# Performance work log

Measured on AMD Instinct MI355X. Metric: run time of the kernel, lower is better.

Reference implementation:

```python
import jax, jax.numpy as jnp
import numpy as np

N_NODES = 50000
N_EDGES = 1600000
IN_C = 256
HID_C = 128
OUT_C = 16
HEADS = 8
NEG_SLOPE = 0.2  # PyG GATConv default


def gat_layer(x, src, dst, W, att_src, att_dst, bias, heads, out_c):
    """PyG-style GATConv (eval mode, add_self_loops already applied to src/dst).
    x: [N, F_in], W: [F_in, heads*out_c], att_*: [heads, out_c], bias: [heads*out_c].
    Returns concatenated heads: [N, heads*out_c]."""
    N = x.shape[0]
    h = (x @ W).reshape(N, heads, out_c)                  # [N, H, C]
    a_src = (h * att_src[None]).sum(-1)                   # [N, H]
    a_dst = (h * att_dst[None]).sum(-1)                   # [N, H]
    alpha = a_src[src] + a_dst[dst]                       # [E, H]
    alpha = jax.nn.leaky_relu(alpha, NEG_SLOPE)
    # segment softmax over incoming edges of each destination node
    amax = jax.ops.segment_max(alpha, dst, num_segments=N)  # [N, H]
    alpha = jnp.exp(alpha - jax.lax.stop_gradient(amax)[dst])
    denom = jax.ops.segment_sum(alpha, dst, num_segments=N)  # [N, H]
    w = alpha / denom[dst]                                # [E, H]
    msg = h[src] * w[:, :, None]                          # [E, H, C]
    out = jax.ops.segment_sum(msg, dst, num_segments=N)   # [N, H, C]
    return out.reshape(N, heads * out_c) + bias


def setup_inputs() -> dict:
    key = jax.random.key(0)
    ks = jax.random.split(key, 10)
    x = jax.random.normal(ks[0], (N_NODES, IN_C), dtype=jnp.float32)
    edge_index = jax.random.randint(ks[1], (2, N_EDGES), 0, N_NODES, dtype=jnp.int32)
    c1 = HID_C // HEADS  # 16 per head
    s1 = 1.0 / np.sqrt(IN_C)
    s2 = 1.0 / np.sqrt(HID_C)
    return {
        "x": x,
        "edge_index": edge_index,
        "W1": jax.random.normal(ks[2], (IN_C, HEADS * c1), dtype=jnp.float32) * s1,
        "att_src1": jax.random.normal(ks[3], (HEADS, c1), dtype=jnp.float32) * s1,
        "att_dst1": jax.random.normal(ks[4], (HEADS, c1), dtype=jnp.float32) * s1,
        "bias1": jnp.zeros((HEADS * c1,), dtype=jnp.float32),
        "W2": jax.random.normal(ks[5], (HID_C, OUT_C), dtype=jnp.float32) * s2,
        "att_src2": jax.random.normal(ks[6], (1, OUT_C), dtype=jnp.float32) * s2,
        "att_dst2": jax.random.normal(ks[7], (1, OUT_C), dtype=jnp.float32) * s2,
        "bias2": jnp.zeros((OUT_C,), dtype=jnp.float32),
    }


def reference(x, edge_index, W1, att_src1, att_dst1, bias1, W2, att_src2, att_dst2, bias2):
    N = x.shape[0]
    loop = jnp.arange(N, dtype=edge_index.dtype)
    src = jnp.concatenate([edge_index[0], loop])  # add_self_loops=True (PyG default)
    dst = jnp.concatenate([edge_index[1], loop])
    h = gat_layer(x, src, dst, W1, att_src1, att_dst1, bias1, HEADS, HID_C // HEADS)
    h = jax.nn.relu(h)
    # F.dropout with training=False is identity (eval mode)
    out = gat_layer(h, src, dst, W2, att_src2, att_dst2, bias2, 1, OUT_C)
    return out
```

## Files before the change

kernel.cpp:

```cpp
#include <hip/hip_runtime.h>
#include <hip/hip_bf16.h>


#define NN 50000
#define NE 1600000
#define NBK 196
#define NB_SC 512
#define CHUNK (NE / NB_SC)
#define GB1 782
#define GB2 1563

typedef __attribute__((ext_vector_type(8))) short bf16x8;
typedef __attribute__((ext_vector_type(4))) float f32x4;

__device__ __forceinline__ float lrelu(float x) { return fmaxf(x, 0.2f * x); }

__device__ __forceinline__ float ldf(const void* p, int i, int isbf) {
  return isbf ? __bfloat162float(((const __hip_bfloat16*)p)[i])
              : ((const float*)p)[i];
}
__device__ __forceinline__ short f2bf_bits(float v) {
  __hip_bfloat16 h = __float2bfloat16(v);
  return *reinterpret_cast<short*>(&h);
}
__device__ __forceinline__ float bfs2f(short b) {
  unsigned int u = ((unsigned int)(unsigned short)b) << 16;
  union { unsigned int u; float f; } c; c.u = u; return c.f;
}
__device__ __forceinline__ unsigned short f2h_bits(float v) {
  _Float16 h = (_Float16)v;
  return *reinterpret_cast<unsigned short*>(&h);
}
__device__ __forceinline__ float h2f(unsigned short b) {
  _Float16 h = *reinterpret_cast<_Float16*>(&b);
  return (float)h;
}

#define OFF_H1   ((size_t)0)
#define OFF_H    ((size_t)25600000)
#define OFF_H2   ((size_t)51200000)
#define OFF_AS1  ((size_t)54400000)
#define OFF_AD1  ((size_t)56000000)
#define OFF_AS2  ((size_t)57600000)
#define OFF_AD2  ((size_t)57800000)
#define OFF_CNT  ((size_t)58000000)
#define OFF_OFFS ((size_t)58400000)
#define OFF_CSR  ((size_t)58600000)
#define OFF_WP1  ((size_t)65000000)
#define OFF_BCNT ((size_t)65065536)
#define OFF_BBASE ((size_t)65066560)
#define OFF_FLAG ((size_t)65068608)

__global__ void repack_w1(const void* __restrict__ W1, short* __restrict__ Wp,
                          const unsigned int* __restrict__ xw, int* __restrict__ flag) {
  __shared__ int s[256];
  __shared__ int sf;
  int t = threadIdx.x;
  unsigned int w = xw[t * 97 + 5];
  unsigned int e = (w >> 7) & 0xFF;
  s[t] = (e >= 116 && e <= 138) ? 1 : 0;
  __syncthreads();
  for (int off = 128; off > 0; off >>= 1) {
    if (t < off) s[t] += s[t + off];
    __syncthreads();
  }
  if (t == 0) {
    sf = (s[0] >= 128) ? 1 : 0;
    if (blockIdx.x == 0) *flag = sf;
  }
  __syncthreads();
  int f = sf;
  int i = blockIdx.x * 256 + t;
  int j = i & 7, q = (i >> 3) & 3, c = (i >> 5) & 127, tt = i >> 12;
  int src = (tt * 32 + q * 8 + j) * 128 + c;
  Wp[i] = f ? ((const short*)W1)[src] : f2bf_bits(((const float*)W1)[src]);
}

__global__ __launch_bounds__(256) void fat1(const void* __restrict__ X,
                                            const short* __restrict__ Wp,
                                            short* __restrict__ H1b,
                                            const int* __restrict__ flag,
                                            const int* __restrict__ dst,
                                            int* __restrict__ HB) {
  __shared__ int h[224];
  if (blockIdx.x < GB1) {
    int wave = threadIdx.x >> 6, lane = threadIdx.x & 63;
    int rowbase = blockIdx.x * 64 + wave * 16;
    int l15 = lane & 15, quad = lane >> 4;
    int f = *flag;
    int arow = rowbase + l15;
    if (arow >= NN) arow = NN - 1;
    f32x4 acc[8];
#pragma unroll
    for (int ct = 0; ct < 8; ++ct) acc[ct] = (f32x4){0.f, 0.f, 0.f, 0.f};
    size_t abase = (size_t)arow * 256 + quad * 8;
#pragma unroll
    for (int kt = 0; kt < 8; ++kt) {
      bf16x8 a;
      if (f) {
        a = *(const bf16x8*)((const short*)X + abase + kt * 32);
      } else {
        const float* xp = (const float*)X + abase + kt * 32;
        float4 v0 = *(const float4*)xp, v1 = *(const float4*)(xp + 4);
        a[0] = f2bf_bits(v0.x); a[1] = f2bf_bits(v0.y);
        a[2] = f2bf_bits(v0.z); a[3] = f2bf_bits(v0.w);
        a[4] = f2bf_bits(v1.x); a[5] = f2bf_bits(v1.y);
        a[6] = f2bf_bits(v1.z); a[7] = f2bf_bits(v1.w);
      }
#pragma unroll
      for (int ct = 0; ct < 8; ++ct) {
        bf16x8 b = *(const bf16x8*)(Wp + ((kt * 128 + ct * 16 + l15) * 4 + quad) * 8);
        acc[ct] = __builtin_amdgcn_mfma_f32_16x16x32_bf16(a, b, acc[ct], 0, 0, 0);
      }
    }
    int r0 = rowbase + quad * 4;
#pragma unroll
    for (int ct = 0; ct < 8; ++ct)
#pragma unroll
      for (int r = 0; r < 4; ++r) {
        int row = r0 + r;
        if (row < NN) H1b[(size_t)row * 128 + ct * 16 + l15] = f2bf_bits(acc[ct][r]);
      }
  } else {
    int b = blockIdx.x - GB1;
    int t = threadIdx.x;
    for (int i = t; i < 224; i += 256) h[i] = 0;
    __syncthreads();
    int e0 = b * CHUNK, e1 = e0 + CHUNK;
    for (int e = e0 + t; e < e1; e += 256) atomicAdd(&h[dst[e] >> 8], 1);
    __syncthreads();
    for (int i = t; i < NBK; i += 256) HB[b * NBK + i] = h[i];
  }
}

__global__ __launch_bounds__(256) void fat2(const short* __restrict__ H1b,
                                            const void* __restrict__ as1,
                                            const void* __restrict__ ad1,
                                            float* __restrict__ AS,
                                            float* __restrict__ AD,
                                            const int* __restrict__ flag,
                                            int* __restrict__ HB,
                                            int* __restrict__ total) {
  __shared__ float s_as[128], s_ad[128];
  __shared__ int ts[256];
  int t = threadIdx.x;
  if (blockIdx.x < GB2) {
    int f = *flag;
    if (t < 128) { s_as[t] = ldf(as1, t, f); s_ad[t] = ldf(ad1, t, f); }
    __syncthreads();
    int tid = blockIdx.x * 256 + t;
    if (tid >= NN * 8) return;
    int n = tid >> 3, hh = tid & 7;
    const bf16x8* hp = (const bf16x8*)(H1b + (size_t)n * 128 + hh * 16);
    bf16x8 v0 = hp[0], v1 = hp[1];
    float as = 0.f, ad = 0.f;
#pragma unroll
    for (int i = 0; i < 8; ++i) {
      int b = hh * 16 + i;
      float x0 = bfs2f(v0[i]), x1 = bfs2f(v1[i]);
      as += x0 * s_as[b] + x1 * s_as[b + 8];
      ad += x0 * s_ad[b] + x1 * s_ad[b + 8];
    }
    AS[tid] = as; AD[tid] = ad;
  } else {
    int k = blockIdx.x - GB2;
    int v0 = HB[(t * 2) * NBK + k], v1 = HB[(t * 2 + 1) * NBK + k];
    int s = v0 + v1;
    ts[t] = s;
    __syncthreads();
    for (int off = 1; off < 256; off <<= 1) {
      int a = (t >= off) ? ts[t - off] : 0;
      __syncthreads();
      ts[t] += a;
      __syncthreads();
    }
    int ex = ts[t] - s;
    HB[(t * 2) * NBK + k] = ex;
    HB[(t * 2 + 1) * NBK + k] = ex + v0;
    if (t == 255) total[k] = ts[255];
  }
}

__global__ void scat_scan2(const int* __restrict__ total, int* __restrict__ bbase,
                           int* __restrict__ bcnt) {
  __shared__ int sd[256];
  int t = threadIdx.x;
  int v = (t < NBK) ? total[t] : 0;
  sd[t] = v;
  __syncthreads();
  for (int off = 1; off < 256; off <<= 1) {
    int a = (t >= off) ? sd[t - off] : 0;
    __syncthreads();
    sd[t] += a;
    __syncthreads();
  }
  if (t < NBK) { bbase[t] = sd[t] - v; bcnt[t] = v; }
}

__global__ __launch_bounds__(256) void scat_write(const int* __restrict__ src,
                                                  const int* __restrict__ dst,
                                                  const int* __restrict__ HB,
                                                  const int* __restrict__ bbase,
                                                  unsigned int* __restrict__ EPp) {
  __shared__ int h[224], sc[256], lofs[224], lc[224], gd[224];
  __shared__ unsigned int EB[CHUNK];
  int t = threadIdx.x, b = blockIdx.x;
  for (int i = t; i < 224; i += 256) h[i] = 0;
  __syncthreads();
  int e0 = b * CHUNK, e1 = e0 + CHUNK;
  for (int e = e0 + t; e < e1; e += 256) atomicAdd(&h[dst[e] >> 8], 1);
  __syncthreads();
  int v = (t < NBK) ? h[t] : 0;
  sc[t] = v;
  __syncthreads();
  for (int off = 1; off < 256; off <<= 1) {
    int a = (t >= off) ? sc[t - off] : 0;
    __syncthreads();
    sc[t] += a;
    __syncthreads();
  }
  if (t < NBK) {
    int ex = sc[t] - v;
    lofs[t] = ex; lc[t] = ex;
    gd[t] = bbase[t] + HB[b * NBK + t];
  }
  __syncthreads();
  for (int e = e0 + t; e < e1; e += 256) {
    int d = dst[e];
    int pos = atomicAdd(&lc[d >> 8], 1);
    EB[pos] = ((unsigned int)(d & 255) << 16) | (unsigned int)src[e];
  }
  __syncthreads();
  for (int k = 0; k < NBK; ++k) {
    int len = h[k];
    if (!len) continue;
    int g0 = gd[k], l0 = lofs[k];
    for (int i = t; i < len; i += 256) EPp[g0 + i] = EB[l0 + i];
  }
}

__global__ __launch_bounds__(1024) void bucket_csr(const unsigned int* __restrict__ EPp,
                                                   const int* __restrict__ bcnt,
                                                   const int* __restrict__ bbase,
                                                   int* __restrict__ cnt,
                                                   int* __restrict__ offs,
                                                   unsigned short* __restrict__ csr) {
  __shared__ int h[256], sc[256], lc[256];
  int b = blockIdx.x, t = threadIdx.x;
  int gbase = bbase[b], n = bcnt[b];
  if (t < 256) h[t] = 0;
  __syncthreads();
  for (int i = t; i < n; i += 1024) atomicAdd(&h[(EPp[gbase + i] >> 16) & 255], 1);
  __syncthreads();
  int v = 0;
  if (t < 256) { v = h[t]; sc[t] = v; }
  __syncthreads();
  for (int off = 1; off < 256; off <<= 1) {
    int add = (t >= off && t < 256) ? sc[t - off] : 0;
    __syncthreads();
    if (t < 256) sc[t] += add;
    __syncthreads();
  }
  if (t < 256) {
    int ex = sc[t] - v;
    int node = (b << 8) + t;
    if (node < NN) { cnt[node] = v; offs[node] = gbase + ex; }
    lc[t] = ex;
  }
  __syncthreads();
  for (int i = t; i < n; i += 1024) {
    unsigned int p = EPp[gbase + i];
    int pos = atomicAdd(&lc[(p >> 16) & 255], 1);
    csr[gbase + pos] = (unsigned short)(p & 0xFFFF);
  }
}

__global__ __launch_bounds__(256) void agg1(const short* __restrict__ H1b,
                                            const float* __restrict__ AS,
                                            const float* __restrict__ AD,
                                            const int* __restrict__ offs,
                                            const int* __restrict__ cnt,
                                            const unsigned short* __restrict__ csr,
                                            const void* __restrict__ bias1,
                                            short* __restrict__ Hb,
                                            const int* __restrict__ flag) {
  int lane = threadIdx.x & 63;
  int node = blockIdx.x * 4 + (threadIdx.x >> 6);
  int f = *flag;
  int start = offs[node], deg = cnt[node];
  int g = lane >> 3, k = lane & 7;
  float adst = AD[node * 8 + k];
  float acc[16];
#pragma unroll
  for (int i = 0; i < 16; ++i) acc[i] = 0.f;
  float dsum = 0.f;
  if (g == 0) {
    float p = __expf(lrelu(AS[node * 8 + k] + adst));
    dsum = p;
    const bf16x8* hp = (const bf16x8*)(H1b + (size_t)node * 128 + k * 16);
    bf16x8 v0 = hp[0], v1 = hp[1];
#pragma unroll
    for (int i = 0; i < 8; ++i) {
      acc[i] = p * bfs2f(v0[i]);
      acc[8 + i] = p * bfs2f(v1[i]);
    }
  }
  int s = (g < deg) ? (int)csr[start + g] : -1;
  float a_c = 0.f; bf16x8 v0, v1;
  if (s >= 0) {
    a_c = AS[s * 8 + k];
    const bf16x8* hp = (const bf16x8*)(H1b + (size_t)s * 128 + k * 16);
    v0 = hp[0]; v1 = hp[1];
  }
  for (int eb = 0; eb < deg; eb += 8) {
    int en = eb + 8 + g;
    int sn = (en < deg) ? (int)csr[start + en] : -1;
    float a_n = 0.f; bf16x8 w0, w1;
    if (sn >= 0) {
      a_n = AS[sn * 8 + k];
      const bf16x8* hp = (const bf16x8*)(H1b + (size_t)sn * 128 + k * 16);
      w0 = hp[0]; w1 = hp[1];
    }
    if (s >= 0) {
      float p = __expf(lrelu(a_c + adst));
      dsum += p;
#pragma unroll
      for (int i = 0; i < 8; ++i) {
        acc[i] += p * bfs2f(v0[i]);
        acc[8 + i] += p * bfs2f(v1[i]);
      }
    }
    s = sn; a_c = a_n; v0 = w0; v1 = w1;
  }
#pragma unroll
  for (int i = 0; i < 16; ++i) {
    acc[i] += __shfl_xor(acc[i], 8);
    acc[i] += __shfl_xor(acc[i], 16);
    acc[i] += __shfl_xor(acc[i], 32);
  }
  dsum += __shfl_xor(dsum, 8);
  dsum += __shfl_xor(dsum, 16);
  dsum += __shfl_xor(dsum, 32);
  if (g == 0) {
    float inv = 1.0f / dsum;
    int c0 = k * 16;
    bf16x8 o0, o1;
#pragma unroll
    for (int i = 0; i < 8; ++i) {
      o0[i] = f2bf_bits(fmaxf(acc[i] * inv + ldf(bias1, c0 + i, f), 0.f));
      o1[i] = f2bf_bits(fmaxf(acc[8 + i] * inv + ldf(bias1, c0 + 8 + i, f), 0.f));
    }
    *(bf16x8*)(Hb + (size_t)node * 128 + c0) = o0;
    *(bf16x8*)(Hb + (size_t)node * 128 + c0 + 8) = o1;
  }
}

__global__ __launch_bounds__(256) void gemm2_a2(const short* __restrict__ Hb,
                                                const void* __restrict__ W2,
                                                const void* __restrict__ as2,
                                                const void* __restrict__ ad2,
                                                unsigned short* __restrict__ H2h,
                                                float* __restrict__ AS2,
                                                float* __restrict__ AD2,
                                                const int* __restrict__ flag) {
  __shared__ float sW[2048];
  __shared__ float s_as[16], s_ad[16];
  int t = threadIdx.x;
  int f = *flag;
  for (int i = t; i < 2048; i += 256) sW[i] = ldf(W2, i, f);
  if (t < 16) { s_as[t] = ldf(as2, t, f); s_ad[t] = ldf(ad2, t, f); }
  __syncthreads();
  int n = blockIdx.x * 16 + (t >> 4), c = t & 15;
  const bf16x8* hp = (const bf16x8*)(Hb + (size_t)n * 128);
  float acc = 0.f;
#pragma unroll 4
  for (int k8 = 0; k8 < 16; ++k8) {
    bf16x8 v = hp[k8];
#pragma unroll
    for (int i = 0; i < 8; ++i) acc += bfs2f(v[i]) * sW[(k8 * 8 + i) * 16 + c];
  }
  H2h[n * 16 + c] = f2h_bits(acc);
  float vs = acc * s_as[c], vd = acc * s_ad[c];
#pragma unroll
  for (int off = 1; off < 16; off <<= 1) {
    vs += __shfl_xor(vs, off);
    vd += __shfl_xor(vd, off);
  }
  if (c == 0) { AS2[n] = vs; AD2[n] = vd; }
}

__global__ __launch_bounds__(256) void agg2(const unsigned short* __restrict__ H2h,
                                            const float* __restrict__ AS2,
                                            const float* __restrict__ AD2,
                                            const int* __restrict__ offs,
                                            const int* __restrict__ cnt,
                                            const unsigned short* __restrict__ csr,
                                            const void* __restrict__ bias2,
                                            void* __restrict__ outv,
                                            const int* __restrict__ flag) {
  int lane = threadIdx.x & 63;
  int node = blockIdx.x * 4 + (threadIdx.x >> 6);
  int f = *flag;
  int start = offs[node], deg = cnt[node];
  int g = lane >> 3, k = lane & 7;
  float adst = AD2[node];
  float a0 = 0.f, a1 = 0.f, dsum = 0.f;
  if (g == 0) {
    float p = __expf(lrelu(AS2[node] + adst));
    dsum = p;
    unsigned int hv = *(const unsigned int*)(H2h + (size_t)node * 16 + k * 2);
    a0 = p * h2f((unsigned short)(hv & 0xFFFF));
    a1 = p * h2f((unsigned short)(hv >> 16));
  }
  int s = (g < deg) ? (int)csr[start + g] : -1;
  float as_c = 0.f; unsigned int hv_c = 0;
  if (s >= 0) {
    as_c = AS2[s];
    hv_c = *(const unsigned int*)(H2h + (size_t)s * 16 + k * 2);
  }
  for (int eb = 0; eb < deg; eb += 8) {
    int en = eb + 8 + g;
    int sn = (en < deg) ? (int)csr[start + en] : -1;
    float as_n = 0.f; unsigned int hv_n = 0;
    if (sn >= 0) {
      as_n = AS2[sn];
      hv_n = *(const unsigned int*)(H2h + (size_t)sn * 16 + k * 2);
    }
    if (s >= 0) {
      float p = __expf(lrelu(as_c + adst));
      dsum += p;
      a0 += p * h2f((unsigned short)(hv_c & 0xFFFF));
      a1 += p * h2f((unsigned short)(hv_c >> 16));
    }
    s = sn; as_c = as_n; hv_c = hv_n;
  }
  a0 += __shfl_xor(a0, 8);  a0 += __shfl_xor(a0, 16);  a0 += __shfl_xor(a0, 32);
  a1 += __shfl_xor(a1, 8);  a1 += __shfl_xor(a1, 16);  a1 += __shfl_xor(a1, 32);
  dsum += __shfl_xor(dsum, 8); dsum += __shfl_xor(dsum, 16); dsum += __shfl_xor(dsum, 32);
  if (g == 0) {
    float inv = 1.0f / dsum;
    float o0 = a0 * inv + ldf(bias2, k * 2 + 0, f);
    float o1 = a1 * inv + ldf(bias2, k * 2 + 1, f);
    size_t base = (size_t)node * 16 + k * 2;
    if (f) {
      ((__hip_bfloat16*)outv)[base] = __float2bfloat16(o0);
      ((__hip_bfloat16*)outv)[base + 1] = __float2bfloat16(o1);
    } else {
      *(float2*)((float*)outv + base) = make_float2(o0, o1);
    }
  }
}

extern "C" void kernel_launch(void* const* d_in, const int* in_sizes, int n_in,
                              void* d_out, int out_size, void* d_ws, size_t ws_size,
                              hipStream_t stream) {
  const void* x = d_in[0];
  const int* ei = (const int*)d_in[1];
  const void* W1 = d_in[2];
  const void* as1 = d_in[3];
  const void* ad1 = d_in[4];
  const void* b1 = d_in[5];
  const void* W2 = d_in[6];
  const void* as2 = d_in[7];
  const void* ad2 = d_in[8];
  const void* b2 = d_in[9];
  char* ws = (char*)d_ws;

  short* H1b = (short*)(ws + OFF_H1);
  short* Hb = (short*)(ws + OFF_H);
  unsigned int* EPp = (unsigned int*)(ws + OFF_H);
  unsigned short* H2h = (unsigned short*)(ws + OFF_H2);
  int* HB = (int*)(ws + OFF_H2);
  float* AS1 = (float*)(ws + OFF_AS1);
  float* AD1 = (float*)(ws + OFF_AD1);
  float* AS2 = (float*)(ws + OFF_AS2);
  float* AD2 = (float*)(ws + OFF_AD2);
  int* CNT = (int*)(ws + OFF_CNT);
  int* OFFS = (int*)(ws + OFF_OFFS);
  unsigned short* CSR = (unsigned short*)(ws + OFF_CSR);
  short* Wp = (short*)(ws + OFF_WP1);
  int* BCNT = (int*)(ws + OFF_BCNT);
  int* BBASE = (int*)(ws + OFF_BBASE);
  int* FLAG = (int*)(ws + OFF_FLAG);

  repack_w1<<<128, 256, 0, stream>>>(W1, Wp, (const unsigned int*)x, FLAG);
  fat1<<<GB1 + NB_SC, 256, 0, stream>>>(x, Wp, H1b, FLAG, ei + NE, HB);
  fat2<<<GB2 + NBK, 256, 0, stream>>>(H1b, as1, ad1, AS1, AD1, FLAG, HB, BCNT);
  scat_scan2<<<1, 256, 0, stream>>>(BCNT, BBASE, BCNT);
  scat_write<<<NB_SC, 256, 0, stream>>>(ei, ei + NE, HB, BBASE, EPp);
  bucket_csr<<<NBK, 1024, 0, stream>>>(EPp, BCNT, BBASE, CNT, OFFS, CSR);

  agg1<<<NN / 4, 256, 0, stream>>>(H1b, AS1, AD1, OFFS, CNT, CSR, b1, Hb, FLAG);
  gemm2_a2<<<NN / 16, 256, 0, stream>>>(Hb, W2, as2, ad2, H2h, AS2, AD2, FLAG);
  agg2<<<NN / 4, 256, 0, stream>>>(H2h, AS2, AD2, OFFS, CNT, CSR, b2, d_out, FLAG);
}
```

Before: 306.0 us.

## Remove scat_scan2 launch and flatten scat_write copy-out loop

Drops the single-block scan kernel and has each block of scat_write and bucket_csr recompute the 196-entry bucket-total prefix scan redundantly in shared memory, which saves one kernel launch and its serialization point. scat_write also records each edge's bucket in a shared byte array, so the final copy to global memory becomes one flat loop over positions instead of a serial loop over 196 buckets with a short inner loop each. The cost is redundant scan work in every block, extra shared memory for the bucket array, and an extra indirection per copied element.

```diff
diff --git a/kernel.cpp b/kernel.cpp
--- a/kernel.cpp
+++ b/kernel.cpp
@@ -47,8 +47,7 @@
 #define OFF_OFFS ((size_t)58400000)
 #define OFF_CSR  ((size_t)58600000)
 #define OFF_WP1  ((size_t)65000000)
-#define OFF_BCNT ((size_t)65065536)
-#define OFF_BBASE ((size_t)65066560)
+#define OFF_TOT  ((size_t)65065536)
 #define OFF_FLAG ((size_t)65068608)
 
 __global__ void repack_w1(const void* __restrict__ W1, short* __restrict__ Wp,
@@ -181,30 +180,25 @@
   }
 }
 
-__global__ void scat_scan2(const int* __restrict__ total, int* __restrict__ bbase,
-                           int* __restrict__ bcnt) {
-  __shared__ int sd[256];
-  int t = threadIdx.x;
-  int v = (t < NBK) ? total[t] : 0;
-  sd[t] = v;
-  __syncthreads();
-  for (int off = 1; off < 256; off <<= 1) {
-    int a = (t >= off) ? sd[t - off] : 0;
-    __syncthreads();
-    sd[t] += a;
-    __syncthreads();
-  }
-  if (t < NBK) { bbase[t] = sd[t] - v; bcnt[t] = v; }
-}
-
 __global__ __launch_bounds__(256) void scat_write(const int* __restrict__ src,
                                                   const int* __restrict__ dst,
                                                   const int* __restrict__ HB,
-                                                  const int* __restrict__ bbase,
+                                                  const int* __restrict__ total,
                                                   unsigned int* __restrict__ EPp) {
   __shared__ int h[224], sc[256], lofs[224], lc[224], gd[224];
   __shared__ unsigned int EB[CHUNK];
+  __shared__ unsigned char BKT[CHUNK];
   int t = threadIdx.x, b = blockIdx.x;
+  int tv = (t < NBK) ? total[t] : 0;
+  sc[t] = tv;
+  __syncthreads();
+  for (int off = 1; off < 256; off <<= 1) {
+    int a = (t >= off) ? sc[t - off] : 0;
+    __syncthreads();
+    sc[t] += a;
+    __syncthreads();
+  }
+  if (t < NBK) gd[t] = (sc[t] - tv) + HB[b * NBK + t];
   for (int i = t; i < 224; i += 256) h[i] = 0;
   __syncthreads();
   int e0 = b * CHUNK, e1 = e0 + CHUNK;
@@ -219,35 +213,42 @@
     sc[t] += a;
     __syncthreads();
   }
-  if (t < NBK) {
-    int ex = sc[t] - v;
-    lofs[t] = ex; lc[t] = ex;
-    gd[t] = bbase[t] + HB[b * NBK + t];
-  }
+  if (t < NBK) { int ex = sc[t] - v; lofs[t] = ex; lc[t] = ex; }
   __syncthreads();
   for (int e = e0 + t; e < e1; e += 256) {
     int d = dst[e];
-    int pos = atomicAdd(&lc[d >> 8], 1);
+    int k = d >> 8;
+    int pos = atomicAdd(&lc[k], 1);
     EB[pos] = ((unsigned int)(d & 255) << 16) | (unsigned int)src[e];
-  }
-  __syncthreads();
-  for (int k = 0; k < NBK; ++k) {
-    int len = h[k];
-    if (!len) continue;
-    int g0 = gd[k], l0 = lofs[k];
-    for (int i = t; i < len; i += 256) EPp[g0 + i] = EB[l0 + i];
+    BKT[pos] = (unsigned char)k;
+  }
+  __syncthreads();
+  for (int pos = t; pos < CHUNK; pos += 256) {
+    int k = BKT[pos];
+    EPp[gd[k] + (pos - lofs[k])] = EB[pos];
   }
 }
 
 __global__ __launch_bounds__(1024) void bucket_csr(const unsigned int* __restrict__ EPp,
-                                                   const int* __restrict__ bcnt,
-                                                   const int* __restrict__ bbase,
+                                                   const int* __restrict__ total,
                                                    int* __restrict__ cnt,
                                                    int* __restrict__ offs,
                                                    unsigned short* __restrict__ csr) {
   __shared__ int h[256], sc[256], lc[256];
   int b = blockIdx.x, t = threadIdx.x;
-  int gbase = bbase[b], n = bcnt[b];
+  int tv = 0;
+  if (t < 256) { tv = (t < NBK) ? total[t] : 0; sc[t] = tv; }
+  __syncthreads();
+  for (int off = 1; off < 256; off <<= 1) {
+    int a = (t >= off && t < 256) ? sc[t - off] : 0;
+    __syncthreads();
+    if (t < 256) sc[t] += a;
+    __syncthreads();
+  }
+  __shared__ int s_gbase, s_n;
+  if (t == (unsigned)b) { s_gbase = sc[b] - tv; s_n = tv; }
+  __syncthreads();
+  int gbase = s_gbase, n = s_n;
   if (t < 256) h[t] = 0;
   __syncthreads();
   for (int i = t; i < n; i += 1024) atomicAdd(&h[(EPp[gbase + i] >> 16) & 255], 1);
@@ -479,16 +480,14 @@
   int* OFFS = (int*)(ws + OFF_OFFS);
   unsigned short* CSR = (unsigned short*)(ws + OFF_CSR);
   short* Wp = (short*)(ws + OFF_WP1);
-  int* BCNT = (int*)(ws + OFF_BCNT);
-  int* BBASE = (int*)(ws + OFF_BBASE);
+  int* TOT = (int*)(ws + OFF_TOT);
   int* FLAG = (int*)(ws + OFF_FLAG);
 
   repack_w1<<<128, 256, 0, stream>>>(W1, Wp, (const unsigned int*)x, FLAG);
   fat1<<<GB1 + NB_SC, 256, 0, stream>>>(x, Wp, H1b, FLAG, ei + NE, HB);
-  fat2<<<GB2 + NBK, 256, 0, stream>>>(H1b, as1, ad1, AS1, AD1, FLAG, HB, BCNT);
-  scat_scan2<<<1, 256, 0, stream>>>(BCNT, BBASE, BCNT);
-  scat_write<<<NB_SC, 256, 0, stream>>>(ei, ei + NE, HB, BBASE, EPp);
-  bucket_csr<<<NBK, 1024, 0, stream>>>(EPp, BCNT, BBASE, CNT, OFFS, CSR);
+  fat2<<<GB2 + NBK, 256, 0, stream>>>(H1b, as1, ad1, AS1, AD1, FLAG, HB, TOT);
+  scat_write<<<NB_SC, 256, 0, stream>>>(ei, ei + NE, HB, TOT, EPp);
+  bucket_csr<<<NBK, 1024, 0, stream>>>(EPp, TOT, CNT, OFFS, CSR);
 
   agg1<<<NN / 4, 256, 0, stream>>>(H1b, AS1, AD1, OFFS, CNT, CSR, b1, Hb, FLAG);
   gemm2_a2<<<NN / 16, 256, 0, stream>>>(Hb, W2, as2, ad2, H2h, AS2, AD2, FLAG);
```

Measured after the change: 273.4 us. 10.6% less time.
